# Optimization experiments

Measured on AMD Instinct MI355X. Metric: run time of the kernel, lower is better.

The kernel has to match this reference:

```python
import jax, jax.numpy as jnp
import numpy as np

TOP_K = 2

def setup_inputs() -> dict:
    key = jax.random.key(0)
    ks = jax.random.split(key, 6)
    B, L, D, E = 4, 4096, 1024, 8
    s = 1.0 / np.sqrt(D)
    return {
        "x": jax.random.normal(ks[0], (B, L, D), dtype=jnp.float32),
        "Wr": jax.random.normal(ks[1], (E, D), dtype=jnp.float32) * s,
        "W1": jax.random.normal(ks[2], (E, D, D), dtype=jnp.float32) * s,
        "b1": jax.random.normal(ks[3], (E, D), dtype=jnp.float32) * 0.01,
        "W2": jax.random.normal(ks[4], (E, D, D), dtype=jnp.float32) * s,
        "b2": jax.random.normal(ks[5], (E, D), dtype=jnp.float32) * 0.01,
    }

def reference(x, Wr, W1, b1, W2, b2):
    # x: [B,L,D]; Wr: [E,D]; W1/W2: [E,D,D]; b1/b2: [E,D]
    E = Wr.shape[0]
    logits = jnp.einsum("bld,ed->ble", x, Wr)           # router, no bias
    probs = jax.nn.softmax(logits, axis=-1)
    topw, topi = jax.lax.top_k(probs, TOP_K)             # [B,L,K]
    topw = topw / jnp.sum(topw, axis=-1, keepdims=True)  # renormalize
    # combine weights per expert: [B,L,E], zero where expert not selected
    comb = jnp.sum(jax.nn.one_hot(topi, E, dtype=x.dtype) * topw[..., None], axis=-2)
    out = jnp.zeros_like(x)
    for e in range(E):  # small fixed expert count
        h = jax.nn.gelu(jnp.einsum("bld,fd->blf", x, W1[e]) + b1[e], approximate=False)
        y = jnp.einsum("blf,df->bld", h, W2[e]) + b2[e]
        out = out + comb[..., e:e + 1] * y
    return out
```

## Files before the change

kernel.cpp:

```cpp
#include <hip/hip_runtime.h>
#include <hip/hip_bf16.h>
#include <cstdint>
#include <cstddef>

#define NTOK 16384
#define DDIM 1024
#define NEXP 8
#define NPAIR 64
#define CPAD 32

typedef __attribute__((ext_vector_type(8))) short bf16x8;
typedef __attribute__((ext_vector_type(4))) float f32x4;

__device__ __forceinline__ unsigned short f2bf(float f) {
  union { float f; unsigned u; } c; c.f = f;
  unsigned r = (c.u + 0x7FFFu + ((c.u >> 16) & 1u)) >> 16;
  return (unsigned short)r;
}

__device__ __forceinline__ float gelu_exact(float v) {
  return 0.5f * v * (1.0f + erff(v * 0.70710678118654752440f));
}

#define GL2LDS(gp, lp) __builtin_amdgcn_global_load_lds( \
    (__attribute__((address_space(1))) void*)(gp),       \
    (__attribute__((address_space(3))) void*)(lp), 16, 0, 0)

__global__ void castw_k(const float* __restrict__ W1, const float* __restrict__ W2,
                        unsigned short* __restrict__ w1b, unsigned short* __restrict__ w2b) {
  const int H = 2 * 1024 * 1024;
  int i = blockIdx.x * blockDim.x + threadIdx.x;
  const float4* s; unsigned short* d; int k;
  if (i < H) { s = (const float4*)W1; d = w1b; k = i; }
  else       { s = (const float4*)W2; d = w2b; k = i - H; }
  float4 a = s[k];
  union { unsigned short s4[4]; uint2 v; } o;
  o.s4[0] = f2bf(a.x); o.s4[1] = f2bf(a.y); o.s4[2] = f2bf(a.z); o.s4[3] = f2bf(a.w);
  ((uint2*)d)[k] = o.v;
}

__global__ __launch_bounds__(256)
void castx_router_k(const float* __restrict__ x, const float* __restrict__ Wr,
                    unsigned short* __restrict__ xb, int* __restrict__ tokP,
                    float2* __restrict__ tokW) {
  const int t = blockIdx.x;
  const int tid = threadIdx.x;
  const int w = tid >> 6, lane = tid & 63;

  float4 xv = ((const float4*)x)[(size_t)t * 256 + tid];
  union { unsigned short s4[4]; uint2 v; } o;
  o.s4[0] = f2bf(xv.x); o.s4[1] = f2bf(xv.y); o.s4[2] = f2bf(xv.z); o.s4[3] = f2bf(xv.w);
  ((uint2*)xb)[(size_t)t * 256 + tid] = o.v;

  const float4* Wr4 = (const float4*)Wr;
  float p[NEXP];
#pragma unroll
  for (int e = 0; e < NEXP; ++e) {
    float4 wv = Wr4[e * 256 + tid];
    p[e] = xv.x * wv.x + xv.y * wv.y + xv.z * wv.z + xv.w * wv.w;
  }
#pragma unroll
  for (int e = 0; e < NEXP; ++e) {
    float v = p[e];
#pragma unroll
    for (int off = 32; off >= 1; off >>= 1) v += __shfl_xor(v, off, 64);
    p[e] = v;
  }
  __shared__ float red[4][NEXP];
  if (lane == 0) {
#pragma unroll
    for (int e = 0; e < NEXP; ++e) red[w][e] = p[e];
  }
  __syncthreads();
  if (tid == 0) {
    float s[NEXP];
#pragma unroll
    for (int e = 0; e < NEXP; ++e) s[e] = red[0][e] + red[1][e] + red[2][e] + red[3][e];
    int e1 = 0; float m1 = s[0];
#pragma unroll
    for (int e = 1; e < NEXP; ++e) if (s[e] > m1) { m1 = s[e]; e1 = e; }
    int e2 = -1; float m2 = -3.4e38f;
#pragma unroll
    for (int e = 0; e < NEXP; ++e) {
      if (e == e1) continue;
      if (s[e] > m2) { m2 = s[e]; e2 = e; }
    }
    float dd = expf(m2 - m1);
    float w1 = 1.f / (1.f + dd);
    float w2 = dd / (1.f + dd);
    int lo = e1 < e2 ? e1 : e2;
    int hi = e1 < e2 ? e2 : e1;
    float wlo = (e1 < e2) ? w1 : w2;
    float whi = (e1 < e2) ? w2 : w1;
    tokP[t] = lo * 8 + hi;
    tokW[t] = make_float2(wlo, whi);
  }
}

__global__ __launch_bounds__(256)
void hist_k(const int* __restrict__ tokP, int* __restrict__ cnt) {
  __shared__ int bins[NPAIR];
  if (threadIdx.x < NPAIR) bins[threadIdx.x] = 0;
  __syncthreads();
  int t = blockIdx.x * 256 + threadIdx.x;
  atomicAdd(&bins[tokP[t]], 1);
  __syncthreads();
  if (threadIdx.x < NPAIR) {
    int c = bins[threadIdx.x];
    if (c) atomicAdd(&cnt[threadIdx.x * CPAD], c);
  }
}

__global__ void offsets_k(const int* __restrict__ cnt, int* __restrict__ off,
                          int* __restrict__ map, int* __restrict__ nwork) {
  if (threadIdx.x == 0) {
    int a = 0, nw = 0;
    for (int s = 0; s < NPAIR; ++s) {
      off[s] = a;
      int c = cnt[s * CPAD];
      a += c;
      for (int mt = 0; mt * 128 < c; ++mt) map[nw++] = (s << 16) | mt;
    }
    nwork[0] = nw;
  }
}

__global__ __launch_bounds__(256)
void place_k(const int* __restrict__ tokP, const float2* __restrict__ tokW,
             const int* __restrict__ off, int* __restrict__ cur,
             int* __restrict__ asgT, float2* __restrict__ asgW2) {
  int t = blockIdx.x * 256 + threadIdx.x;
  int pid = tokP[t];
  int lane = threadIdx.x & 63;
  int slot = 0;
#pragma unroll 1
  for (int s = 0; s < NPAIR; ++s) {
    unsigned long long m = __ballot(pid == s);
    if (pid == s) {
      int leader = __ffsll((long long)m) - 1;
      int base = 0;
      if (lane == leader) base = atomicAdd(&cur[s * CPAD], (int)__popcll(m));
      base = __shfl(base, leader, 64);
      slot = base + (int)__popcll(m & ((1ull << lane) - 1ull));
    }
  }
  int p = off[pid] + slot;
  asgT[p] = t;
  asgW2[p] = tokW[t];
}


__global__ __launch_bounds__(256)
void gemm1_k(const unsigned short* __restrict__ xb, const unsigned short* __restrict__ w1b,
             const float* __restrict__ b1, const int* __restrict__ cntp,
             const int* __restrict__ offp, const int* __restrict__ map,
             const int* __restrict__ nwork, const int* __restrict__ asgT,
             const float2* __restrict__ asgW2, unsigned short* __restrict__ h) {
  if ((int)blockIdx.x >= nwork[0]) return;
  const int mp = map[blockIdx.x];
  const int pid = mp >> 16, mt = mp & 0xFFFF;
  const int cnt = cntp[pid * CPAD];
  const int off = offp[pid];
  const int m0 = mt * 128;
  const int n0 = blockIdx.y * 128;
  const int half = n0 >> 10;
  const int e = half ? (pid & 7) : (pid >> 3);
  const int nc0 = n0 & 1023;

  __shared__ __align__(16) unsigned short As[2][4096];
  __shared__ __align__(16) unsigned short Bs[2][4096];

  const int tid = threadIdx.x;
  const int w = tid >> 6, lane = tid & 63;
  const int r = lane & 15, kc = lane >> 4;
  const int wr = w >> 1, wc = w & 1;

  const unsigned short* srcA[2];
  const unsigned short* srcB[2];
#pragma unroll
  for (int i = 0; i < 2; ++i) {
    int g = w + i * 4;
    int rowt = m0 + g * 16 + r;
    int rowc = (rowt < cnt) ? rowt : m0;
    int tok = asgT[off + rowc];
    srcA[i] = xb + (size_t)tok * DDIM + kc * 8;
    int coln = nc0 + g * 16 + r;
    srcB[i] = w1b + (size_t)e * DDIM * DDIM + (size_t)coln * DDIM + kc * 8;
  }

  f32x4 acc[4][4];
#pragma unroll
  for (int i = 0; i < 4; ++i)
#pragma unroll
    for (int j = 0; j < 4; ++j) acc[i][j] = (f32x4){0.f, 0.f, 0.f, 0.f};

  auto stage = [&](int buf, int k0) {
#pragma unroll
    for (int i = 0; i < 2; ++i) {
      int g = w + i * 4;
      GL2LDS(srcA[i] + k0, &As[buf][g * 512 + lane * 8]);
      GL2LDS(srcB[i] + k0, &Bs[buf][g * 512 + lane * 8]);
    }
  };

  stage(0, 0);
#pragma unroll 2
  for (int t = 0; t < 32; ++t) {
    int buf = t & 1;
    __syncthreads();
    if (t + 1 < 32) stage(buf ^ 1, (t + 1) * 32);
    bf16x8 af[4], bv[4];
#pragma unroll
    for (int i = 0; i < 4; ++i) {
      af[i] = *(const bf16x8*)&As[buf][(wr * 4 + i) * 512 + lane * 8];
      bv[i] = *(const bf16x8*)&Bs[buf][(wc * 4 + i) * 512 + lane * 8];
    }
#pragma unroll
    for (int i = 0; i < 4; ++i)
#pragma unroll
      for (int j = 0; j < 4; ++j)
        acc[i][j] = __builtin_amdgcn_mfma_f32_16x16x32_bf16(af[i], bv[j], acc[i][j], 0, 0, 0);
  }

  float bcol[4];
#pragma unroll
  for (int j = 0; j < 4; ++j) bcol[j] = b1[e * DDIM + nc0 + wc * 64 + j * 16 + r];
#pragma unroll
  for (int i = 0; i < 4; ++i) {
#pragma unroll
    for (int q = 0; q < 4; ++q) {
      int grow = m0 + wr * 64 + i * 16 + kc * 4 + q;
      if (grow < cnt) {
        float2 wv = asgW2[off + grow];
        float sc = half ? wv.y : wv.x;
        size_t hrow = (size_t)(off + grow) * 2048;
#pragma unroll
        for (int j = 0; j < 4; ++j) {
          int col = n0 + wc * 64 + j * 16 + r;
          h[hrow + col] = f2bf(sc * gelu_exact(acc[i][j][q] + bcol[j]));
        }
      }
    }
  }
}

__global__ __launch_bounds__(256)
void gemm2_k(const unsigned short* __restrict__ hsrc, const unsigned short* __restrict__ w2b,
             const float* __restrict__ b2, const int* __restrict__ cntp,
             const int* __restrict__ offp, const int* __restrict__ map,
             const int* __restrict__ nwork, const int* __restrict__ asgT,
             const float2* __restrict__ asgW2, float* __restrict__ out) {
  if ((int)blockIdx.x >= nwork[0]) return;
  const int mp = map[blockIdx.x];
  const int pid = mp >> 16, mt = mp & 0xFFFF;
  const int cnt = cntp[pid * CPAD];
  const int off = offp[pid];
  const int m0 = mt * 128;
  const int n0 = blockIdx.y * 128;
  const int elo = pid >> 3, ehi = pid & 7;

  __shared__ __align__(16) unsigned short As[2][8192];
  __shared__ __align__(16) unsigned short Bs[2][8192];

  const int tid = threadIdx.x;
  const int w = tid >> 6, lane = tid & 63;
  const int r = lane & 15, kc = lane >> 4;
  const int wr = w >> 1, wc = w & 1;

  const unsigned short* srcA[2];
  const unsigned short* srcBlo[2];
  const unsigned short* srcBhi[2];
#pragma unroll
  for (int i = 0; i < 2; ++i) {
    int g = w + i * 4;
    int rowt = m0 + g * 16 + r;
    int rowc = (rowt < cnt) ? rowt : m0;
    srcA[i] = hsrc + (size_t)(off + rowc) * 2048 + kc * 8;
    int coln = n0 + g * 16 + r;
    srcBlo[i] = w2b + (size_t)elo * DDIM * DDIM + (size_t)coln * DDIM + kc * 8;
    srcBhi[i] = w2b + (size_t)ehi * DDIM * DDIM + (size_t)coln * DDIM + kc * 8;
  }

  f32x4 acc[4][4];
#pragma unroll
  for (int i = 0; i < 4; ++i)
#pragma unroll
    for (int j = 0; j < 4; ++j) acc[i][j] = (f32x4){0.f, 0.f, 0.f, 0.f};

  auto stage = [&](int buf, int k0) {
    int kb = k0 & 1023;
#pragma unroll
    for (int i = 0; i < 2; ++i) {
      int g = w + i * 4;
      const unsigned short* pb = (k0 & 1024) ? srcBhi[i] : srcBlo[i];
#pragma unroll
      for (int ks = 0; ks < 2; ++ks) {
        GL2LDS(srcA[i] + k0 + ks * 32, &As[buf][(g * 2 + ks) * 512 + lane * 8]);
        GL2LDS(pb + kb + ks * 32,      &Bs[buf][(g * 2 + ks) * 512 + lane * 8]);
      }
    }
  };

  stage(0, 0);
  for (int t = 0; t < 32; ++t) {
    int buf = t & 1;
    __syncthreads();
    if (t + 1 < 32) stage(buf ^ 1, (t + 1) * 64);
#pragma unroll
    for (int ks = 0; ks < 2; ++ks) {
      bf16x8 af[4], bv[4];
#pragma unroll
      for (int i = 0; i < 4; ++i) {
        af[i] = *(const bf16x8*)&As[buf][((wr * 4 + i) * 2 + ks) * 512 + lane * 8];
        bv[i] = *(const bf16x8*)&Bs[buf][((wc * 4 + i) * 2 + ks) * 512 + lane * 8];
      }
#pragma unroll
      for (int i = 0; i < 4; ++i)
#pragma unroll
        for (int j = 0; j < 4; ++j)
          acc[i][j] = __builtin_amdgcn_mfma_f32_16x16x32_bf16(af[i], bv[j], acc[i][j], 0, 0, 0);
    }
  }

  float b2lo[4], b2hi[4];
#pragma unroll
  for (int j = 0; j < 4; ++j) {
    int col = n0 + wc * 64 + j * 16 + r;
    b2lo[j] = b2[elo * DDIM + col];
    b2hi[j] = b2[ehi * DDIM + col];
  }
#pragma unroll
  for (int i = 0; i < 4; ++i) {
#pragma unroll
    for (int q = 0; q < 4; ++q) {
      int grow = m0 + wr * 64 + i * 16 + kc * 4 + q;
      if (grow < cnt) {
        int tok = asgT[off + grow];
        float2 wv = asgW2[off + grow];
        float* orow = out + (size_t)tok * DDIM;
#pragma unroll
        for (int j = 0; j < 4; ++j) {
          int col = n0 + wc * 64 + j * 16 + r;
          orow[col] = acc[i][j][q] + wv.x * b2lo[j] + wv.y * b2hi[j];
        }
      }
    }
  }
}

extern "C" void kernel_launch(void* const* d_in, const int* in_sizes, int n_in,
                              void* d_out, int out_size, void* d_ws, size_t ws_size,
                              hipStream_t stream) {
  (void)in_sizes; (void)n_in; (void)ws_size; (void)out_size;
  const float* x  = (const float*)d_in[0];
  const float* Wr = (const float*)d_in[1];
  const float* W1 = (const float*)d_in[2];
  const float* b1 = (const float*)d_in[3];
  const float* W2 = (const float*)d_in[4];
  const float* b2 = (const float*)d_in[5];
  float* out = (float*)d_out;

  char* ws = (char*)d_ws;
  int*    cnt   = (int*)(ws + 0);
  int*    cur   = (int*)(ws + 8192);
  int*    off   = (int*)(ws + 16384);
  int*    nwork = (int*)(ws + 16640);
  int*    map   = (int*)(ws + 16648);
  int*    tokP  = (int*)(ws + 32768);
  float2* tokW  = (float2*)(ws + 98304);
  int*    asgT  = (int*)(ws + 229376);
  float2* asgW2 = (float2*)(ws + 294912);
  unsigned short* xb  = (unsigned short*)(ws + (size_t)(1u << 20));
  unsigned short* w1b = (unsigned short*)(ws + (size_t)33 * (1u << 20));
  unsigned short* w2b = (unsigned short*)(ws + (size_t)49 * (1u << 20));
  unsigned short* h   = (unsigned short*)(ws + (size_t)65 * (1u << 20));

  hipMemsetAsync(ws, 0, 16384, stream);

  castw_k<<<16384, 256, 0, stream>>>(W1, W2, w1b, w2b);
  castx_router_k<<<NTOK, 256, 0, stream>>>(x, Wr, xb, tokP, tokW);
  hist_k<<<NTOK / 256, 256, 0, stream>>>(tokP, cnt);
  offsets_k<<<1, 64, 0, stream>>>(cnt, off, map, nwork);
  place_k<<<NTOK / 256, 256, 0, stream>>>(tokP, tokW, off, cur, asgT, asgW2);

  dim3 g1(160, 16);
  dim3 g2(160, 8);
  gemm1_k<<<g1, 256, 0, stream>>>(xb, w1b, b1, cnt, off, map, nwork, asgT, asgW2, h);
  gemm2_k<<<g2, 256, 0, stream>>>(h, w2b, b2, cnt, off, map, nwork, asgT, asgW2, out);
}
```

Baseline: 682.5 us.

## Remap GEMM blocks per XCD, deepen gemm1 K-stage, skip empty pair ballots

Block indices in both grouped GEMMs are remapped so that consecutive logical tiles land on the same XCD, which aims to improve L2 reuse of shared weight and activation tiles. gemm1 now stages 64 K-elements per pipeline step instead of 32, halving the number of barriers at the cost of doubling its LDS footprint. place_k skips pair iterations whose ballot is empty. Higher LDS use may lower occupancy for gemm1.

```diff
diff --git a/kernel.cpp b/kernel.cpp
--- a/kernel.cpp
+++ b/kernel.cpp
@@ -25,6 +25,12 @@
 #define GL2LDS(gp, lp) __builtin_amdgcn_global_load_lds( \
     (__attribute__((address_space(1))) void*)(gp),       \
     (__attribute__((address_space(3))) void*)(lp), 16, 0, 0)
+
+__device__ __forceinline__ int xcd_chunk(int lin, int n) {
+  int q = n >> 3, r = n & 7;
+  int xcd = lin & 7, pos = lin >> 3;
+  return (xcd < r) ? (xcd * (q + 1) + pos) : (r * (q + 1) + (xcd - r) * q + pos);
+}
 
 __global__ void castw_k(const float* __restrict__ W1, const float* __restrict__ W2,
                         unsigned short* __restrict__ w1b, unsigned short* __restrict__ w2b) {
@@ -136,6 +142,7 @@
 #pragma unroll 1
   for (int s = 0; s < NPAIR; ++s) {
     unsigned long long m = __ballot(pid == s);
+    if (!m) continue;
     if (pid == s) {
       int leader = __ffsll((long long)m) - 1;
       int base = 0;
@@ -156,19 +163,22 @@
              const int* __restrict__ offp, const int* __restrict__ map,
              const int* __restrict__ nwork, const int* __restrict__ asgT,
              const float2* __restrict__ asgW2, unsigned short* __restrict__ h) {
-  if ((int)blockIdx.x >= nwork[0]) return;
-  const int mp = map[blockIdx.x];
+  const int nl = xcd_chunk(blockIdx.x + blockIdx.y * gridDim.x, gridDim.x * gridDim.y);
+  const int bx = nl % gridDim.x;
+  const int by = nl / gridDim.x;
+  if (bx >= nwork[0]) return;
+  const int mp = map[bx];
   const int pid = mp >> 16, mt = mp & 0xFFFF;
   const int cnt = cntp[pid * CPAD];
   const int off = offp[pid];
   const int m0 = mt * 128;
-  const int n0 = blockIdx.y * 128;
+  const int n0 = by * 128;
   const int half = n0 >> 10;
   const int e = half ? (pid & 7) : (pid >> 3);
   const int nc0 = n0 & 1023;
 
-  __shared__ __align__(16) unsigned short As[2][4096];
-  __shared__ __align__(16) unsigned short Bs[2][4096];
+  __shared__ __align__(16) unsigned short As[2][8192];
+  __shared__ __align__(16) unsigned short Bs[2][8192];
 
   const int tid = threadIdx.x;
   const int w = tid >> 6, lane = tid & 63;
@@ -198,28 +208,33 @@
 #pragma unroll
     for (int i = 0; i < 2; ++i) {
       int g = w + i * 4;
-      GL2LDS(srcA[i] + k0, &As[buf][g * 512 + lane * 8]);
-      GL2LDS(srcB[i] + k0, &Bs[buf][g * 512 + lane * 8]);
+#pragma unroll
+      for (int ks = 0; ks < 2; ++ks) {
+        GL2LDS(srcA[i] + k0 + ks * 32, &As[buf][(g * 2 + ks) * 512 + lane * 8]);
+        GL2LDS(srcB[i] + k0 + ks * 32, &Bs[buf][(g * 2 + ks) * 512 + lane * 8]);
+      }
     }
   };
 
   stage(0, 0);
-#pragma unroll 2
-  for (int t = 0; t < 32; ++t) {
+  for (int t = 0; t < 16; ++t) {
     int buf = t & 1;
     __syncthreads();
-    if (t + 1 < 32) stage(buf ^ 1, (t + 1) * 32);
-    bf16x8 af[4], bv[4];
-#pragma unroll
-    for (int i = 0; i < 4; ++i) {
-      af[i] = *(const bf16x8*)&As[buf][(wr * 4 + i) * 512 + lane * 8];
-      bv[i] = *(const bf16x8*)&Bs[buf][(wc * 4 + i) * 512 + lane * 8];
-    }
-#pragma unroll
-    for (int i = 0; i < 4; ++i)
-#pragma unroll
-      for (int j = 0; j < 4; ++j)
-        acc[i][j] = __builtin_amdgcn_mfma_f32_16x16x32_bf16(af[i], bv[j], acc[i][j], 0, 0, 0);
+    if (t + 1 < 16) stage(buf ^ 1, (t + 1) * 64);
+#pragma unroll
+    for (int ks = 0; ks < 2; ++ks) {
+      bf16x8 af[4], bv[4];
+#pragma unroll
+      for (int i = 0; i < 4; ++i) {
+        af[i] = *(const bf16x8*)&As[buf][((wr * 4 + i) * 2 + ks) * 512 + lane * 8];
+        bv[i] = *(const bf16x8*)&Bs[buf][((wc * 4 + i) * 2 + ks) * 512 + lane * 8];
+      }
+#pragma unroll
+      for (int i = 0; i < 4; ++i)
+#pragma unroll
+        for (int j = 0; j < 4; ++j)
+          acc[i][j] = __builtin_amdgcn_mfma_f32_16x16x32_bf16(af[i], bv[j], acc[i][j], 0, 0, 0);
+    }
   }
 
   float bcol[4];
@@ -250,13 +265,16 @@
              const int* __restrict__ offp, const int* __restrict__ map,
              const int* __restrict__ nwork, const int* __restrict__ asgT,
              const float2* __restrict__ asgW2, float* __restrict__ out) {
-  if ((int)blockIdx.x >= nwork[0]) return;
-  const int mp = map[blockIdx.x];
+  const int nl = xcd_chunk(blockIdx.x + blockIdx.y * gridDim.x, gridDim.x * gridDim.y);
+  const int bx = nl % gridDim.x;
+  const int by = nl / gridDim.x;
+  if (bx >= nwork[0]) return;
+  const int mp = map[bx];
   const int pid = mp >> 16, mt = mp & 0xFFFF;
   const int cnt = cntp[pid * CPAD];
   const int off = offp[pid];
   const int m0 = mt * 128;
-  const int n0 = blockIdx.y * 128;
+  const int n0 = by * 128;
   const int elo = pid >> 3, ehi = pid & 7;
 
   __shared__ __align__(16) unsigned short As[2][8192];
```

Result: no change. 691.2 us (+1.3%).
